# Optimization experiments

Hardware: AMD Instinct MI355X
Metric: run time of the kernel (lower is better)

Reference implementation:

```python
import jax, jax.numpy as jnp
import numpy as np

N = 100000
E = 1600000
DIM = 64
HEADS = 8
HEAD_DIM = DIM // HEADS
LN_EPS = 1e-5
NORM_EPS = 1e-12


def setup_inputs() -> dict:
    key = jax.random.key(0)
    ks = jax.random.split(key, 5)
    x = jax.random.normal(ks[0], (N, DIM), dtype=jnp.float32)
    edge_index = jax.random.randint(ks[1], (2, E), 0, N, dtype=jnp.int32)
    W_w = jax.random.normal(ks[2], (DIM, DIM), dtype=jnp.float32) * (1.0 / np.sqrt(DIM))
    W_b = jax.random.normal(ks[3], (DIM,), dtype=jnp.float32) * 0.01
    a = jax.random.normal(ks[4], (HEADS, 2 * HEAD_DIM), dtype=jnp.float32) * 0.1
    ln_scale = jnp.ones((DIM,), dtype=jnp.float32)
    ln_bias = jnp.zeros((DIM,), dtype=jnp.float32)
    return {"x": x, "edge_index": edge_index, "W_w": W_w, "W_b": W_b,
            "a": a, "ln_scale": ln_scale, "ln_bias": ln_bias}


def reference(x, edge_index, W_w, W_b, a, ln_scale, ln_bias):
    n = x.shape[0]
    # Linear (dropout = identity in eval), reshape to heads
    h = (x @ W_w.T + W_b).reshape(n, HEADS, HEAD_DIM)          # [N,H,D]
    src, dst = edge_index[0], edge_index[1]
    hs = h[src]                                                 # [E,H,D]
    hd = h[dst]                                                 # [E,H,D]
    a_src, a_dst = a[:, :HEAD_DIM], a[:, HEAD_DIM:]             # [H,D] each
    # (a * cat(hs, hd)).sum(-1) split over the two halves
    alpha = jnp.einsum('ehd,hd->eh', hs, a_src) + jnp.einsum('ehd,hd->eh', hd, a_dst)
    alpha = jnp.where(alpha >= 0, alpha, 0.2 * alpha)           # LeakyReLU(0.2)
    alpha = jax.nn.softmax(alpha, axis=1)                       # NOTE: over heads, as in source
    msg = alpha[..., None] * hd                                 # [E,H,D]
    out = jax.ops.segment_sum(msg, src, num_segments=n)         # scatter-add to src nodes
    out = out.reshape(n, DIM)
    # residual + LayerNorm
    y = out + x
    mu = jnp.mean(y, axis=-1, keepdims=True)
    var = jnp.mean((y - mu) ** 2, axis=-1, keepdims=True)
    y = (y - mu) * jax.lax.rsqrt(var + LN_EPS) * ln_scale + ln_bias
    # F.normalize(p=2, dim=-1)
    norm = jnp.sqrt(jnp.sum(y * y, axis=-1, keepdims=True))
    return y / jnp.maximum(norm, NORM_EPS)
```

## Files before the change

kernel.cpp:

```cpp
#include <hip/hip_runtime.h>
#include <hip/hip_fp16.h>
#include <math.h>

#define N_NODES 100000
#define N_EDGES 1600000
#define LN_EPS 1e-5f
#define NORM_EPS 1e-12f
#define ROWS_PER_BLOCK 32
#define GEMM_BLOCKS (N_NODES / ROWS_PER_BLOCK)
#define WSTRIDE 66
#define WB 64
#define NBKT ((N_NODES + WB - 1) / WB)
#define BIN_TILE 8192
#define BIN_BLOCKS ((N_EDGES + BIN_TILE - 1) / BIN_TILE)
#define GB_LDS 25088
#define CAP 1280

__global__ __launch_bounds__(256) void k_gemm_bin(
    const float* __restrict__ x, const float* __restrict__ W,
    const float* __restrict__ b, const float* __restrict__ a,
    __half* __restrict__ h16,
    float* __restrict__ s_src, float* __restrict__ s_dst,
    const int* __restrict__ ei, int* __restrict__ gbin,
    unsigned int* __restrict__ staged)
{
    extern __shared__ char smem[];
    const int tid = threadIdx.x;

    if (blockIdx.x < BIN_BLOCKS) {
        int* hist = (int*)smem;
        int* base = hist + NBKT;
        for (int bb = tid; bb < NBKT; bb += 256) hist[bb] = 0;
        __syncthreads();

        const int e0 = blockIdx.x * BIN_TILE;
        #pragma unroll 4
        for (int j = 0; j < 32; ++j) {
            const int e = e0 + j * 256 + tid;
            if (e < N_EDGES) atomicAdd(&hist[ei[e] >> 6], 1);
        }
        __syncthreads();
        for (int bb = tid; bb < NBKT; bb += 256)
            if (hist[bb]) base[bb] = atomicAdd(&gbin[bb], hist[bb]);
        __syncthreads();
        #pragma unroll 4
        for (int j = 0; j < 32; ++j) {
            const int e = e0 + j * 256 + tid;
            if (e < N_EDGES) {
                const int s = ei[e];
                const int d = ei[N_EDGES + e];
                const int idx = atomicAdd(&base[s >> 6], 1);
                staged[(size_t)idx] = (unsigned int)((s & 63) | (d << 6));
            }
        }
        return;
    }

    float* WL = (float*)smem;
    float* xs = WL + 64 * WSTRIDE;
    const int lane = tid & 63;
    const int wv   = tid >> 6;

    for (int idx = tid * 4; idx < 64 * 64; idx += 256 * 4) {
        const float4 w = *(const float4*)(W + idx);
        const int c = idx >> 6, k = idx & 63;
        WL[c * WSTRIDE + k + 0] = w.x;
        WL[c * WSTRIDE + k + 1] = w.y;
        WL[c * WSTRIDE + k + 2] = w.z;
        WL[c * WSTRIDE + k + 3] = w.w;
    }
    const int row0 = (blockIdx.x - BIN_BLOCKS) * ROWS_PER_BLOCK;
    for (int idx = tid * 4; idx < ROWS_PER_BLOCK * 64; idx += 256 * 4)
        *(float4*)(xs + idx) = *(const float4*)(x + (size_t)row0 * 64 + idx);
    __syncthreads();

    const float bias = b[lane];
    float acc[8];
    #pragma unroll
    for (int r = 0; r < 8; ++r) acc[r] = bias;

    const int rbase = wv * 8;
    const float* wrow = WL + lane * WSTRIDE;
    const float* xrow = xs + rbase * 64;
    #pragma unroll 1
    for (int kk = 0; kk < 64; kk += 4) {
        const float2 w01 = *(const float2*)(wrow + kk);
        const float2 w23 = *(const float2*)(wrow + kk + 2);
        #pragma unroll
        for (int r = 0; r < 8; ++r) {
            const float4 xq = *(const float4*)(xrow + r * 64 + kk);
            acc[r] += xq.x * w01.x + xq.y * w01.y + xq.z * w23.x + xq.w * w23.y;
        }
    }

    const float asrc = a[(lane >> 3) * 16 + (lane & 7)];
    const float adst = a[(lane >> 3) * 16 + 8 + (lane & 7)];
    #pragma unroll
    for (int r = 0; r < 8; ++r) {
        const int row = row0 + rbase + r;
        const float v = acc[r];
        h16[(size_t)row * 64 + lane] = __float2half_rn(v);
        float p = v * asrc, q = v * adst;
        p += __shfl_xor(p, 1);  q += __shfl_xor(q, 1);
        p += __shfl_xor(p, 2);  q += __shfl_xor(q, 2);
        p += __shfl_xor(p, 4);  q += __shfl_xor(q, 4);
        if ((lane & 7) == 0) {
            s_src[row * 8 + (lane >> 3)] = p;
            s_dst[row * 8 + (lane >> 3)] = q;
        }
    }
}

__global__ __launch_bounds__(1024) void k_hist(
    const int* __restrict__ ei, int* __restrict__ bhist)
{
    __shared__ int hist[NBKT];
    const int tid = threadIdx.x;
    for (int b = tid; b < NBKT; b += 1024) hist[b] = 0;
    __syncthreads();
    const int e0 = blockIdx.x * BIN_TILE;
    #pragma unroll
    for (int j = 0; j < 8; ++j) {
        const int e = e0 + j * 1024 + tid;
        if (e < N_EDGES) atomicAdd(&hist[ei[e] >> 6], 1);
    }
    __syncthreads();
    for (int b = tid; b < NBKT; b += 1024)
        if (hist[b]) atomicAdd(&bhist[b], hist[b]);
}

__global__ __launch_bounds__(1024) void k_bscan(
    const int* __restrict__ bhist, int* __restrict__ bucket_base,
    int* __restrict__ gbin)
{
    __shared__ int wsum[16];
    const int tid = threadIdx.x, lane = tid & 63, wv = tid >> 6;

    int v = (tid < NBKT) ? bhist[tid] : 0;
    int sc = v;
    #pragma unroll
    for (int off = 1; off < 64; off <<= 1) {
        int t = __shfl_up(sc, off);
        if (lane >= off) sc += t;
    }
    if (lane == 63) wsum[wv] = sc;
    __syncthreads();
    if (tid < 16) {
        int ws = wsum[tid];
        #pragma unroll
        for (int off = 1; off < 16; off <<= 1) {
            int t = __shfl_up(ws, off);
            if (tid >= off) ws += t;
        }
        wsum[tid] = ws;
    }
    __syncthreads();
    const int pref0 = wv ? wsum[wv - 1] : 0;
    const int ex0 = pref0 + sc - v;
    if (tid < NBKT) { bucket_base[tid] = ex0; gbin[tid] = ex0; }
    const int T1 = wsum[15];
    __syncthreads();

    const int i2 = 1024 + tid;
    int v2 = (i2 < NBKT) ? bhist[i2] : 0;
    int sc2 = v2;
    #pragma unroll
    for (int off = 1; off < 64; off <<= 1) {
        int t = __shfl_up(sc2, off);
        if (lane >= off) sc2 += t;
    }
    if (lane == 63) wsum[wv] = sc2;
    __syncthreads();
    if (tid < 16) {
        int ws = wsum[tid];
        #pragma unroll
        for (int off = 1; off < 16; off <<= 1) {
            int t = __shfl_up(ws, off);
            if (tid >= off) ws += t;
        }
        wsum[tid] = ws;
    }
    __syncthreads();
    const int pref1 = wv ? wsum[wv - 1] : 0;
    const int ex1 = T1 + pref1 + sc2 - v2;
    if (i2 < NBKT) { bucket_base[i2] = ex1; gbin[i2] = ex1; }
    if (tid == 0) bucket_base[NBKT] = N_EDGES;
}

__global__ __launch_bounds__(1024) void k_place_gather(
    const int* __restrict__ bucket_base, const unsigned int* __restrict__ staged,
    const float* __restrict__ s_src, const float* __restrict__ s_dst,
    const __half* __restrict__ h16, const float* __restrict__ x,
    const float* __restrict__ ln_scale, const float* __restrict__ ln_bias,
    int* __restrict__ dst_ovf, __half* __restrict__ alpha_ovf,
    float* __restrict__ out)
{
    __shared__ int lrow[WB + 1];
    __shared__ int cur[WB];
    __shared__ unsigned int dstl[CAP];
    __shared__ uint4 alds[CAP];

    const int g   = blockIdx.x;
    const int n0  = g * WB;
    const int tid = threadIdx.x;
    if (tid < WB) cur[tid] = 0;
    __syncthreads();
    const int beg = bucket_base[g];
    const int end = bucket_base[g + 1];

    for (int j = beg + tid; j < end; j += 1024)
        atomicAdd(&cur[staged[j] & 63u], 1);
    __syncthreads();
    if (tid < WB) {
        const int c = cur[tid];
        int sc = c;
        #pragma unroll
        for (int off = 1; off < 64; off <<= 1) {
            int t = __shfl_up(sc, off);
            if (tid >= off) sc += t;
        }
        lrow[tid] = sc - c;
        cur[tid]  = sc - c;
        if (tid == WB - 1) lrow[WB] = sc;
    }
    __syncthreads();

    for (int j = beg + tid; j < end; j += 1024) {
        const unsigned int w = staged[j];
        const int srcl = (int)(w & 63u);
        const int dst  = (int)(w >> 6);

        const float4 a0 = *(const float4*)(s_src + (size_t)(n0 + srcl) * 8);
        const float4 a1 = *(const float4*)(s_src + (size_t)(n0 + srcl) * 8 + 4);
        const float4 b0 = *(const float4*)(s_dst + (size_t)dst * 8);
        const float4 b1 = *(const float4*)(s_dst + (size_t)dst * 8 + 4);
        float sc[8] = {a0.x + b0.x, a0.y + b0.y, a0.z + b0.z, a0.w + b0.w,
                       a1.x + b1.x, a1.y + b1.y, a1.z + b1.z, a1.w + b1.w};
        float m = -1e30f;
        #pragma unroll
        for (int h = 0; h < 8; ++h) {
            sc[h] = (sc[h] >= 0.f) ? sc[h] : 0.2f * sc[h];
            m = fmaxf(m, sc[h]);
        }
        float sum = 0.f;
        #pragma unroll
        for (int h = 0; h < 8; ++h) { sc[h] = __expf(sc[h] - m); sum += sc[h]; }
        const float inv = 1.f / sum;
        unsigned int q[4];
        #pragma unroll
        for (int jj = 0; jj < 4; ++jj) {
            const unsigned short lo = __half_as_ushort(__float2half_rn(sc[2*jj]   * inv));
            const unsigned short hi = __half_as_ushort(__float2half_rn(sc[2*jj+1] * inv));
            q[jj] = (unsigned int)lo | ((unsigned int)hi << 16);
        }

        const int ls = atomicAdd(&cur[srcl], 1);
        if (ls < CAP) {
            dstl[ls] = (unsigned int)dst;
            alds[ls] = make_uint4(q[0], q[1], q[2], q[3]);
        } else {
            dst_ovf[beg + ls] = dst;
            *(uint4*)(alpha_ovf + (size_t)(beg + ls) * 8) =
                make_uint4(q[0], q[1], q[2], q[3]);
        }
    }
    __syncthreads();

    const int lane = tid & 63;
    const int wv   = tid >> 6;
    const int head = lane >> 3;

    #pragma unroll 1
    for (int r = 0; r < 4; ++r) {
        const int nl = wv * 4 + r;
        const int i  = n0 + nl;
        if (i >= N_NODES) continue;
        const int bl = lrow[nl];
        const int el = lrow[nl + 1];
        const float xres = x[(size_t)i * 64 + lane];

        float acc = 0.f;
        if (el <= CAP) {
            int e = bl;
            for (; e + 7 < el; e += 8) {
                int d[8];
                #pragma unroll
                for (int j = 0; j < 8; ++j)
                    d[j] = __builtin_amdgcn_readfirstlane((int)dstl[e + j]);
                float al[8];
                #pragma unroll
                for (int j = 0; j < 8; ++j)
                    al[j] = __half2float(((const __half*)&alds[e + j])[head]);
                float hv[8];
                #pragma unroll
                for (int j = 0; j < 8; ++j)
                    hv[j] = __half2float(h16[(size_t)d[j] * 64 + lane]);
                #pragma unroll
                for (int j = 0; j < 8; ++j) acc = fmaf(al[j], hv[j], acc);
            }
            for (; e + 3 < el; e += 4) {
                int d[4];
                #pragma unroll
                for (int j = 0; j < 4; ++j)
                    d[j] = __builtin_amdgcn_readfirstlane((int)dstl[e + j]);
                float al[4];
                #pragma unroll
                for (int j = 0; j < 4; ++j)
                    al[j] = __half2float(((const __half*)&alds[e + j])[head]);
                float hv[4];
                #pragma unroll
                for (int j = 0; j < 4; ++j)
                    hv[j] = __half2float(h16[(size_t)d[j] * 64 + lane]);
                #pragma unroll
                for (int j = 0; j < 4; ++j) acc = fmaf(al[j], hv[j], acc);
            }
            for (; e < el; ++e) {
                const int d = __builtin_amdgcn_readfirstlane((int)dstl[e]);
                acc = fmaf(__half2float(((const __half*)&alds[e])[head]),
                           __half2float(h16[(size_t)d * 64 + lane]), acc);
            }
        } else {
            for (int e = bl; e < el; ++e) {
                int d; float al;
                if (e < CAP) {
                    d  = (int)dstl[e];
                    al = __half2float(((const __half*)&alds[e])[head]);
                } else {
                    d  = dst_ovf[beg + e];
                    al = __half2float(alpha_ovf[(size_t)(beg + e) * 8 + head]);
                }
                acc = fmaf(al, __half2float(h16[(size_t)d * 64 + lane]), acc);
            }
        }

        float v = acc + xres;
        float s = v;
        #pragma unroll
        for (int off = 1; off < 64; off <<= 1) s += __shfl_xor(s, off);
        const float mu = s * (1.f / 64.f);
        const float dd = v - mu;
        float vs = dd * dd;
        #pragma unroll
        for (int off = 1; off < 64; off <<= 1) vs += __shfl_xor(vs, off);
        const float var = vs * (1.f / 64.f);
        float y = dd * rsqrtf(var + LN_EPS) * ln_scale[lane] + ln_bias[lane];
        float ss = y * y;
        #pragma unroll
        for (int off = 1; off < 64; off <<= 1) ss += __shfl_xor(ss, off);
        const float norm = sqrtf(ss);
        out[(size_t)i * 64 + lane] = y / fmaxf(norm, NORM_EPS);
    }
}

extern "C" void kernel_launch(void* const* d_in, const int* in_sizes, int n_in,
                              void* d_out, int out_size, void* d_ws, size_t ws_size,
                              hipStream_t stream)
{
    const float* x        = (const float*)d_in[0];
    const int*   ei       = (const int*)d_in[1];
    const float* W        = (const float*)d_in[2];
    const float* b        = (const float*)d_in[3];
    const float* a        = (const float*)d_in[4];
    const float* ln_scale = (const float*)d_in[5];
    const float* ln_bias  = (const float*)d_in[6];
    float* out = (float*)d_out;

    char* ws = (char*)d_ws;
    size_t off = 0;
    auto alloc = [&](size_t bytes) {
        void* p = ws + off;
        off = (off + bytes + 255) & ~(size_t)255;
        return p;
    };
    __half* h16        = (__half*)alloc((size_t)N_NODES * 64 * 2);
    float*  s_src      = (float*) alloc((size_t)N_NODES * 8 * 4);
    float*  s_dst      = (float*) alloc((size_t)N_NODES * 8 * 4);
    int*    bhist      = (int*)   alloc((size_t)NBKT * 4);
    int*    bucket_base= (int*)   alloc((size_t)(NBKT + 1) * 4);
    int*    gbin       = (int*)   alloc((size_t)NBKT * 4);
    unsigned int* staged = (unsigned int*)alloc((size_t)N_EDGES * 4);
    int*    dst_ovf    = (int*)   alloc((size_t)N_EDGES * 4);
    __half* alpha_ovf  = (__half*)alloc((size_t)N_EDGES * 8 * 2);

    hipMemsetAsync(bhist, 0, (size_t)NBKT * 4, stream);

    k_hist        <<<BIN_BLOCKS, 1024, 0, stream>>>(ei, bhist);
    k_bscan       <<<1, 1024, 0, stream>>>(bhist, bucket_base, gbin);
    k_gemm_bin    <<<BIN_BLOCKS + GEMM_BLOCKS, 256, GB_LDS, stream>>>(
        x, W, b, a, h16, s_src, s_dst, ei, gbin, staged);
    k_place_gather<<<NBKT, 1024, 0, stream>>>(bucket_base, staged, s_src, s_dst,
                                              h16, x, ln_scale, ln_bias,
                                              dst_ovf, alpha_ovf, out);
}
```

Before: 204.8 us.

## Replace per-source CSR sort with LDS float atomic accumulation per bucket

Drops the in-block counting sort of edges by local source node (count atomics, scan, placement into dstl). Each wave now takes a contiguous slice of the bucket's edges in staged order and adds alpha*h into a 64x64 shared-memory accumulator with LDS float atomics. This removes a pass over staged, two barriers and the dst overflow buffer, and CAP is raised. In exchange every edge element costs an LDS atomic instead of a register FMA, and the order of float summation becomes nondeterministic.

```diff
diff --git a/kernel.cpp b/kernel.cpp
--- a/kernel.cpp
+++ b/kernel.cpp
@@ -14,7 +14,7 @@
 #define BIN_TILE 8192
 #define BIN_BLOCKS ((N_EDGES + BIN_TILE - 1) / BIN_TILE)
 #define GB_LDS 25088
-#define CAP 1280
+#define CAP 1536
 
 __global__ __launch_bounds__(256) void k_gemm_bin(
     const float* __restrict__ x, const float* __restrict__ W,
@@ -192,38 +192,20 @@
     const float* __restrict__ s_src, const float* __restrict__ s_dst,
     const __half* __restrict__ h16, const float* __restrict__ x,
     const float* __restrict__ ln_scale, const float* __restrict__ ln_bias,
-    int* __restrict__ dst_ovf, __half* __restrict__ alpha_ovf,
-    float* __restrict__ out)
-{
-    __shared__ int lrow[WB + 1];
-    __shared__ int cur[WB];
-    __shared__ unsigned int dstl[CAP];
+    __half* __restrict__ alpha_ovf, float* __restrict__ out)
+{
+    __shared__ float accs[WB * 64];
     __shared__ uint4 alds[CAP];
 
     const int g   = blockIdx.x;
     const int n0  = g * WB;
     const int tid = threadIdx.x;
-    if (tid < WB) cur[tid] = 0;
-    __syncthreads();
     const int beg = bucket_base[g];
     const int end = bucket_base[g + 1];
-
-    for (int j = beg + tid; j < end; j += 1024)
-        atomicAdd(&cur[staged[j] & 63u], 1);
-    __syncthreads();
-    if (tid < WB) {
-        const int c = cur[tid];
-        int sc = c;
-        #pragma unroll
-        for (int off = 1; off < 64; off <<= 1) {
-            int t = __shfl_up(sc, off);
-            if (tid >= off) sc += t;
-        }
-        lrow[tid] = sc - c;
-        cur[tid]  = sc - c;
-        if (tid == WB - 1) lrow[WB] = sc;
-    }
-    __syncthreads();
+    const int nseg = end - beg;
+
+    #pragma unroll
+    for (int k = tid; k < WB * 64; k += 1024) accs[k] = 0.f;
 
     for (int j = beg + tid; j < end; j += 1024) {
         const unsigned int w = staged[j];
@@ -254,86 +236,69 @@
             q[jj] = (unsigned int)lo | ((unsigned int)hi << 16);
         }
 
-        const int ls = atomicAdd(&cur[srcl], 1);
-        if (ls < CAP) {
-            dstl[ls] = (unsigned int)dst;
+        const int ls = j - beg;
+        if (ls < CAP)
             alds[ls] = make_uint4(q[0], q[1], q[2], q[3]);
-        } else {
-            dst_ovf[beg + ls] = dst;
-            *(uint4*)(alpha_ovf + (size_t)(beg + ls) * 8) =
+        else
+            *(uint4*)(alpha_ovf + (size_t)j * 8) =
                 make_uint4(q[0], q[1], q[2], q[3]);
-        }
     }
     __syncthreads();
 
     const int lane = tid & 63;
     const int wv   = tid >> 6;
     const int head = lane >> 3;
+
+    const int per = (nseg + 15) >> 4;
+    const int w0 = wv * per;
+    const int w1 = min(w0 + per, nseg);
+    const int wc = min(w1, CAP);
+
+    int e = w0;
+    for (; e + 7 < wc; e += 8) {
+        int srcl[8], dst[8];
+        #pragma unroll
+        for (int j = 0; j < 8; ++j) {
+            const unsigned int wj = staged[beg + e + j];
+            srcl[j] = (int)(wj & 63u);
+            dst[j]  = (int)(wj >> 6);
+        }
+        float al[8];
+        #pragma unroll
+        for (int j = 0; j < 8; ++j)
+            al[j] = __half2float(((const __half*)&alds[e + j])[head]);
+        float hv[8];
+        #pragma unroll
+        for (int j = 0; j < 8; ++j)
+            hv[j] = __half2float(h16[(size_t)dst[j] * 64 + lane]);
+        #pragma unroll
+        for (int j = 0; j < 8; ++j)
+            atomicAdd(&accs[srcl[j] * 64 + lane], al[j] * hv[j]);
+    }
+    for (; e < wc; ++e) {
+        const unsigned int wj = staged[beg + e];
+        const int srcl = (int)(wj & 63u);
+        const int dst  = (int)(wj >> 6);
+        const float al = __half2float(((const __half*)&alds[e])[head]);
+        const float hv = __half2float(h16[(size_t)dst * 64 + lane]);
+        atomicAdd(&accs[srcl * 64 + lane], al * hv);
+    }
+    for (e = (w0 > CAP ? w0 : CAP); e < w1; ++e) {
+        const unsigned int wj = staged[beg + e];
+        const int srcl = (int)(wj & 63u);
+        const int dst  = (int)(wj >> 6);
+        const float al = __half2float(alpha_ovf[(size_t)(beg + e) * 8 + head]);
+        const float hv = __half2float(h16[(size_t)dst * 64 + lane]);
+        atomicAdd(&accs[srcl * 64 + lane], al * hv);
+    }
+    __syncthreads();
 
     #pragma unroll 1
     for (int r = 0; r < 4; ++r) {
         const int nl = wv * 4 + r;
         const int i  = n0 + nl;
         if (i >= N_NODES) continue;
-        const int bl = lrow[nl];
-        const int el = lrow[nl + 1];
-        const float xres = x[(size_t)i * 64 + lane];
-
-        float acc = 0.f;
-        if (el <= CAP) {
-            int e = bl;
-            for (; e + 7 < el; e += 8) {
-                int d[8];
-                #pragma unroll
-                for (int j = 0; j < 8; ++j)
-                    d[j] = __builtin_amdgcn_readfirstlane((int)dstl[e + j]);
-                float al[8];
-                #pragma unroll
-                for (int j = 0; j < 8; ++j)
-                    al[j] = __half2float(((const __half*)&alds[e + j])[head]);
-                float hv[8];
-                #pragma unroll
-                for (int j = 0; j < 8; ++j)
-                    hv[j] = __half2float(h16[(size_t)d[j] * 64 + lane]);
-                #pragma unroll
-                for (int j = 0; j < 8; ++j) acc = fmaf(al[j], hv[j], acc);
-            }
-            for (; e + 3 < el; e += 4) {
-                int d[4];
-                #pragma unroll
-                for (int j = 0; j < 4; ++j)
-                    d[j] = __builtin_amdgcn_readfirstlane((int)dstl[e + j]);
-                float al[4];
-                #pragma unroll
-                for (int j = 0; j < 4; ++j)
-                    al[j] = __half2float(((const __half*)&alds[e + j])[head]);
-                float hv[4];
-                #pragma unroll
-                for (int j = 0; j < 4; ++j)
-                    hv[j] = __half2float(h16[(size_t)d[j] * 64 + lane]);
-                #pragma unroll
-                for (int j = 0; j < 4; ++j) acc = fmaf(al[j], hv[j], acc);
-            }
-            for (; e < el; ++e) {
-                const int d = __builtin_amdgcn_readfirstlane((int)dstl[e]);
-                acc = fmaf(__half2float(((const __half*)&alds[e])[head]),
-                           __half2float(h16[(size_t)d * 64 + lane]), acc);
-            }
-        } else {
-            for (int e = bl; e < el; ++e) {
-                int d; float al;
-                if (e < CAP) {
-                    d  = (int)dstl[e];
-                    al = __half2float(((const __half*)&alds[e])[head]);
-                } else {
-                    d  = dst_ovf[beg + e];
-                    al = __half2float(alpha_ovf[(size_t)(beg + e) * 8 + head]);
-                }
-                acc = fmaf(al, __half2float(h16[(size_t)d * 64 + lane]), acc);
-            }
-        }
-
-        float v = acc + xres;
+        float v = accs[nl * 64 + lane] + x[(size_t)i * 64 + lane];
         float s = v;
         #pragma unroll
         for (int off = 1; off < 64; off <<= 1) s += __shfl_xor(s, off);
@@ -379,7 +344,6 @@
     int*    bucket_base= (int*)   alloc((size_t)(NBKT + 1) * 4);
     int*    gbin       = (int*)   alloc((size_t)NBKT * 4);
     unsigned int* staged = (unsigned int*)alloc((size_t)N_EDGES * 4);
-    int*    dst_ovf    = (int*)   alloc((size_t)N_EDGES * 4);
     __half* alpha_ovf  = (__half*)alloc((size_t)N_EDGES * 8 * 2);
 
     hipMemsetAsync(bhist, 0, (size_t)NBKT * 4, stream);
@@ -390,5 +354,5 @@
         x, W, b, a, h16, s_src, s_dst, ei, gbin, staged);
     k_place_gather<<<NBKT, 1024, 0, stream>>>(bucket_base, staged, s_src, s_dst,
                                               h16, x, ln_scale, ln_bias,
-                                              dst_ovf, alpha_ovf, out);
-}
+                                              alpha_ovf, out);
+}
```

New measurement: 743.4 us. 3.63x slower.
